# Kernel optimization log

Hardware: AMD Instinct MI355X
Metric: run time of the kernel (lower is better)

The kernel has to match this reference:

```python
import jax, jax.numpy as jnp
import numpy as np

K = 128   # per-head dim == input dim
H = 8     # heads
B = 2
T = 2048


def setup_inputs() -> dict:
    key = jax.random.key(0)
    ks = jax.random.split(key, 6)
    s_in = 1.0 / np.sqrt(K)
    s_out = 1.0 / np.sqrt(K * H)
    return {
        "x": jax.random.normal(ks[0], (B, T, K), dtype=jnp.float32),
        # Linear weights stored as (in, out); torch Linear init ~ U(-1/sqrt(in), 1/sqrt(in))
        "Wq": jax.random.uniform(ks[1], (K, K * H), jnp.float32, -s_in, s_in),
        "Wk": jax.random.uniform(ks[2], (K, K * H), jnp.float32, -s_in, s_in),
        "Wv": jax.random.uniform(ks[3], (K, K * H), jnp.float32, -s_in, s_in),
        "Wo": jax.random.uniform(ks[4], (K * H, K), jnp.float32, -s_out, s_out),
        "bo": jax.random.uniform(ks[5], (K,), jnp.float32, -s_out, s_out),
    }


def reference(x, Wq, Wk, Wv, Wo, bo):
    b, t, k = x.shape
    h = H
    scale = k ** 0.25
    # projections -> [b, t, h, k]
    q = (x @ Wq).reshape(b, t, h, k) / scale
    ke = (x @ Wk).reshape(b, t, h, k) / scale
    v = (x @ Wv).reshape(b, t, h, k)
    # scores: [b, h, t, t]
    scores = jnp.einsum('bihk,bjhk->bhij', q, ke)
    # causal mask: positions j > i get -inf (diagonal kept)
    causal = jnp.tril(jnp.ones((t, t), dtype=bool))
    scores = jnp.where(causal[None, None], scores, -jnp.inf)
    p = jax.nn.softmax(scores, axis=-1)
    out = jnp.einsum('bhij,bjhk->bihk', p, v).reshape(b, t, h * k)
    return out @ Wo + bo
```

## Files before the change

### kernel.cpp

```cpp
#include <hip/hip_runtime.h>

typedef __bf16 bf16;
typedef __bf16 bf16x4 __attribute__((ext_vector_type(4)));
typedef __bf16 bf16x8 __attribute__((ext_vector_type(8)));
typedef float f32x4 __attribute__((ext_vector_type(4)));

#define MFMA16(a, b, c) __builtin_amdgcn_mfma_f32_16x16x32_bf16((a), (b), (c), 0, 0, 0)

__device__ __forceinline__ int swz16(int r, int c) { return (c ^ (r & 15)); }
__device__ __forceinline__ int swz8(int r, int c) { return (c ^ (r & 7)); }

__global__ __launch_bounds__(256) void tr3_kernel(
    const float* __restrict__ Wq, const float* __restrict__ Wk,
    const float* __restrict__ Wv, bf16* __restrict__ outbase) {
  __shared__ bf16 tile[32][33];
  const int z = blockIdx.z;
  const float* ib = (z == 0) ? Wq : (z == 1) ? Wk : Wv;
  bf16* ob = outbase + (size_t)z * 131072;
  int r0 = blockIdx.x * 32, c0 = blockIdx.y * 32;
  int tx = threadIdx.x & 31, ty = threadIdx.x >> 5;
#pragma unroll
  for (int i = 0; i < 4; ++i) {
    int r = ty + i * 8;
    tile[r][tx] = (bf16)ib[(size_t)(r0 + r) * 1024 + (c0 + tx)];
  }
  __syncthreads();
#pragma unroll
  for (int i = 0; i < 4; ++i) {
    int r = ty + i * 8;
    ob[(size_t)(c0 + r) * 128 + (r0 + tx)] = tile[tx][r];
  }
}

__global__ __launch_bounds__(256) void trWo_kernel(
    const float* __restrict__ in, bf16* __restrict__ out) {
  __shared__ bf16 tile[32][33];
  int r0 = blockIdx.x * 32, c0 = blockIdx.y * 32;
  int tx = threadIdx.x & 31, ty = threadIdx.x >> 5;
#pragma unroll
  for (int i = 0; i < 4; ++i) {
    int r = ty + i * 8;
    tile[r][tx] = (bf16)in[(size_t)(r0 + r) * 128 + (c0 + tx)];
  }
  __syncthreads();
#pragma unroll
  for (int i = 0; i < 4; ++i) {
    int r = ty + i * 8;
    out[(size_t)(c0 + r) * 1024 + (r0 + tx)] = tile[tx][r];
  }
}

__global__ __launch_bounds__(256) void proj_gemm(
    const float* __restrict__ x, const bf16* __restrict__ Wqt,
    const bf16* __restrict__ Wkt, const bf16* __restrict__ Wvt,
    bf16* __restrict__ Qb, bf16* __restrict__ Kb, bf16* __restrict__ Vt) {
  __shared__ __align__(16) bf16 As[128 * 128];
  __shared__ __align__(16) bf16 Bs[128 * 128];
  const int mt = blockIdx.x;
  const int nt = blockIdx.y;
  const int matid = nt >> 3, h = nt & 7;
  const bf16* W = (matid == 0) ? Wqt : (matid == 1) ? Wkt : Wvt;
  const int tid = threadIdx.x;
  const bf16* sb = W + (size_t)h * 128 * 128;
#pragma unroll
  for (int i = 0; i < 8; ++i) {
    int c = tid + i * 256;
    int r = c >> 4, cc = c & 15;
    const f32x4* p = (const f32x4*)(x + (size_t)(mt * 128 + r) * 128 + cc * 8);
    f32x4 a = p[0], b = p[1];
    bf16x8 o;
#pragma unroll
    for (int j = 0; j < 4; ++j) { o[j] = (bf16)a[j]; o[4 + j] = (bf16)b[j]; }
    *(bf16x8*)&As[r * 128 + swz16(r, cc) * 8] = o;
  }
#pragma unroll
  for (int i = 0; i < 8; ++i) {
    int c = tid + i * 256;
    int r = c >> 4, cc = c & 15;
    *(bf16x8*)&Bs[r * 128 + swz16(r, cc) * 8] = *(const bf16x8*)(sb + (size_t)r * 128 + cc * 8);
  }
  __syncthreads();
  const int wave = tid >> 6, lane = tid & 63;
  const int wr = (wave >> 1) * 64, wc = (wave & 1) * 64;
  const int lr = lane & 15, lkb = lane >> 4;
  const f32x4 FZ = {0.f, 0.f, 0.f, 0.f};
  f32x4 acc[4][4];
#pragma unroll
  for (int mf = 0; mf < 4; ++mf)
#pragma unroll
    for (int nf = 0; nf < 4; ++nf) acc[mf][nf] = FZ;
  const bool qk = (matid < 2);
#pragma unroll
  for (int ks = 0; ks < 4; ++ks) {
    bf16x8 a[4], b[4];
#pragma unroll
    for (int mf = 0; mf < 4; ++mf) {
      int r = wr + mf * 16 + lr;
      a[mf] = *(const bf16x8*)&As[r * 128 + swz16(r, ks * 4 + lkb) * 8];
    }
#pragma unroll
    for (int nf = 0; nf < 4; ++nf) {
      int r = wc + nf * 16 + lr;
      b[nf] = *(const bf16x8*)&Bs[r * 128 + swz16(r, ks * 4 + lkb) * 8];
    }
    if (qk) {
#pragma unroll
      for (int mf = 0; mf < 4; ++mf)
#pragma unroll
        for (int nf = 0; nf < 4; ++nf) acc[mf][nf] = MFMA16(b[nf], a[mf], acc[mf][nf]);
    } else {
#pragma unroll
      for (int mf = 0; mf < 4; ++mf)
#pragma unroll
        for (int nf = 0; nf < 4; ++nf) acc[mf][nf] = MFMA16(a[mf], b[nf], acc[mf][nf]);
    }
  }
  const int rb = lkb * 4;
  if (qk) {
    bf16* Out = (matid == 0) ? Qb : Kb;
#pragma unroll
    for (int mf = 0; mf < 4; ++mf)
#pragma unroll
      for (int nf = 0; nf < 4; ++nf) {
        int m = mt * 128 + wr + mf * 16 + lr;
        int d0 = wc + nf * 16 + rb;
        int bb = m >> 11, t = m & 2047;
        bf16x4 vv;
#pragma unroll
        for (int r = 0; r < 4; ++r) vv[r] = (bf16)acc[mf][nf][r];
        *(bf16x4*)(Out + ((size_t)(bb * 8 + h) * 2048 + t) * 128 + d0) = vv;
      }
  } else {
#pragma unroll
    for (int mf = 0; mf < 4; ++mf)
#pragma unroll
      for (int nf = 0; nf < 4; ++nf) {
        int d = wc + nf * 16 + lr;
        int m0 = mt * 128 + wr + mf * 16 + rb;
        int bb = m0 >> 11, t0 = m0 & 2047;
        bf16x4 vv;
#pragma unroll
        for (int r = 0; r < 4; ++r) vv[r] = (bf16)acc[mf][nf][r];
        *(bf16x4*)(Vt + ((size_t)(bb * 8 + h) * 128 + d) * 2048 + t0) = vv;
      }
  }
}

__global__ __launch_bounds__(256, 3) void attn_kernel(
    bf16* __restrict__ Qb, const bf16* __restrict__ Kb, const bf16* __restrict__ Vt) {
  __shared__ __align__(16) bf16 Ks[64 * 128];
  __shared__ __align__(16) bf16 Vs[128 * 64];
  __shared__ __align__(16) bf16 Ps[4 * 16 * 64];
  const f32x4 FZ = {0.f, 0.f, 0.f, 0.f};
  const int bid = blockIdx.x;
  const int qt = 31 - (bid >> 4);
  const int bh = bid & 15;
  const int nT = qt + 1;
  const bf16* Qh = Qb + (size_t)bh * 2048 * 128;
  bf16* Qw = Qb + (size_t)bh * 2048 * 128;
  const bf16* Kh = Kb + (size_t)bh * 2048 * 128;
  const bf16* Vh = Vt + (size_t)bh * 128 * 2048;
  const int tid = threadIdx.x, wave = tid >> 6, lane = tid & 63;
  const int lr = lane & 15, lkb = lane >> 4, rb = lkb * 4;
  const float SCL = 0.12751744f;
  const int qrow = qt * 64 + wave * 16;

  const int krow = tid >> 4, kcc = tid & 15;
  bf16* kdst = &Ks[krow * 128 + (kcc ^ krow) * 8];
  const bf16* ksrc0 = Kh + (size_t)krow * 128 + kcc * 8;
  const int vrow = tid >> 3, vcc = tid & 7;
  bf16* vdst = &Vs[vrow * 64 + (vcc ^ (vrow & 7)) * 8];
  const bf16* vsrc0 = Vh + (size_t)vrow * 2048 + vcc * 8;

  float mrun[4], lrun[4];
  f32x4 O[8];
  bf16x8 qf[4];
#pragma unroll
  for (int r = 0; r < 4; ++r) { mrun[r] = -__builtin_inff(); lrun[r] = 0.f; }
#pragma unroll
  for (int nf = 0; nf < 8; ++nf) O[nf] = FZ;
#pragma unroll
  for (int ks = 0; ks < 4; ++ks)
    qf[ks] = *(const bf16x8*)(Qh + (size_t)(qrow + lr) * 128 + ks * 32 + lkb * 8);

  bf16x8 kpre[4], vpre[4];
#pragma unroll
  for (int i = 0; i < 4; ++i) kpre[i] = *(const bf16x8*)(ksrc0 + i * 2048);
#pragma unroll
  for (int i = 0; i < 4; ++i) vpre[i] = *(const bf16x8*)(vsrc0 + i * 65536);

  for (int it = 0; it < nT; ++it) {
    __syncthreads();
#pragma unroll
    for (int i = 0; i < 4; ++i) *(bf16x8*)(kdst + i * 2048) = kpre[i];
#pragma unroll
    for (int i = 0; i < 4; ++i) *(bf16x8*)(vdst + i * 2048) = vpre[i];
    __syncthreads();
    if (it + 1 < nT) {
      const size_t koff = (size_t)(it + 1) * 8192;
      const size_t voff = (size_t)(it + 1) * 64;
#pragma unroll
      for (int i = 0; i < 4; ++i) kpre[i] = *(const bf16x8*)(ksrc0 + koff + i * 2048);
#pragma unroll
      for (int i = 0; i < 4; ++i) vpre[i] = *(const bf16x8*)(vsrc0 + voff + i * 65536);
    }
    f32x4 s[4];
#pragma unroll
    for (int nf = 0; nf < 4; ++nf) s[nf] = FZ;
#pragma unroll
    for (int ks = 0; ks < 4; ++ks) {
#pragma unroll
      for (int nf = 0; nf < 4; ++nf) {
        int r = nf * 16 + lr;
        bf16x8 b = *(const bf16x8*)&Ks[r * 128 + swz16(r, ks * 4 + lkb) * 8];
        s[nf] = MFMA16(qf[ks], b, s[nf]);
      }
    }
    float pmax[4];
#pragma unroll
    for (int r = 0; r < 4; ++r) pmax[r] = -__builtin_inff();
    if (it == qt) {
#pragma unroll
      for (int nf = 0; nf < 4; ++nf) {
        int colg = (qt << 6) + nf * 16 + lr;
#pragma unroll
        for (int r = 0; r < 4; ++r) {
          int rowg = qrow + rb + r;
          float v = (colg > rowg) ? -__builtin_inff() : s[nf][r];
          s[nf][r] = v;
          pmax[r] = fmaxf(pmax[r], v);
        }
      }
    } else {
#pragma unroll
      for (int nf = 0; nf < 4; ++nf)
#pragma unroll
        for (int r = 0; r < 4; ++r) pmax[r] = fmaxf(pmax[r], s[nf][r]);
    }
#pragma unroll
    for (int r = 0; r < 4; ++r) {
      float v = pmax[r];
      v = fmaxf(v, __shfl_xor(v, 1, 64));
      v = fmaxf(v, __shfl_xor(v, 2, 64));
      v = fmaxf(v, __shfl_xor(v, 4, 64));
      v = fmaxf(v, __shfl_xor(v, 8, 64));
      pmax[r] = v;
    }
    float alpha[4];
#pragma unroll
    for (int r = 0; r < 4; ++r) {
      float mnew = fmaxf(mrun[r], pmax[r] * SCL);
      alpha[r] = exp2f(mrun[r] - mnew);
      mrun[r] = mnew;
    }
    float psum[4] = {0.f, 0.f, 0.f, 0.f};
#pragma unroll
    for (int nf = 0; nf < 4; ++nf)
#pragma unroll
      for (int r = 0; r < 4; ++r) {
        float p = exp2f(__builtin_fmaf(s[nf][r], SCL, -mrun[r]));
        s[nf][r] = p;
        psum[r] += p;
      }
#pragma unroll
    for (int r = 0; r < 4; ++r) {
      float v = psum[r];
      v += __shfl_xor(v, 1, 64);
      v += __shfl_xor(v, 2, 64);
      v += __shfl_xor(v, 4, 64);
      v += __shfl_xor(v, 8, 64);
      lrun[r] = lrun[r] * alpha[r] + v;
    }
#pragma unroll
    for (int nf = 0; nf < 8; ++nf) {
#pragma unroll
      for (int r = 0; r < 4; ++r) O[nf][r] *= alpha[r];
    }
#pragma unroll
    for (int nf = 0; nf < 4; ++nf) {
#pragma unroll
      for (int r = 0; r < 4; ++r) {
        int row = rb + r;
        int col = nf * 16 + lr;
        Ps[wave * 1024 + row * 64 + swz8(row, col >> 3) * 8 + (col & 7)] = (bf16)s[nf][r];
      }
    }
#pragma unroll
    for (int ks2 = 0; ks2 < 2; ++ks2) {
      bf16x8 a = *(const bf16x8*)&Ps[wave * 1024 + lr * 64 + swz8(lr, ks2 * 4 + lkb) * 8];
#pragma unroll
      for (int nf = 0; nf < 8; ++nf) {
        int r = nf * 16 + lr;
        bf16x8 b = *(const bf16x8*)&Vs[r * 64 + swz8(r, ks2 * 4 + lkb) * 8];
        O[nf] = MFMA16(a, b, O[nf]);
      }
    }
  }
#pragma unroll
  for (int r = 0; r < 4; ++r) {
    float inv = 1.f / lrun[r];
    int t = qrow + rb + r;
#pragma unroll
    for (int nf = 0; nf < 8; ++nf)
      Qw[(size_t)t * 128 + nf * 16 + lr] = (bf16)(O[nf][r] * inv);
  }
}

__global__ __launch_bounds__(256) void outproj_kernel(
    const bf16* __restrict__ AO, const bf16* __restrict__ Wot,
    const float* __restrict__ bo, float* __restrict__ out) {
  __shared__ __align__(16) bf16 As[32 * 128];
  __shared__ __align__(16) bf16 Bs[128 * 128];
  const f32x4 FZ = {0.f, 0.f, 0.f, 0.f};
  const int mt = blockIdx.x;
  const int tid = threadIdx.x, wave = tid >> 6, lane = tid & 63;
  const int lr = lane & 15, lkb = lane >> 4, rb = lkb * 4;
  const int wr = (wave >> 1) * 16, wc = (wave & 1) * 64;
  f32x4 acc[4];
#pragma unroll
  for (int nf = 0; nf < 4; ++nf) acc[nf] = FZ;
  for (int kt = 0; kt < 8; ++kt) {
    __syncthreads();
#pragma unroll
    for (int i = 0; i < 2; ++i) {
      int c = tid + i * 256;
      int r = c >> 4, cc = c & 15;
      int m = mt * 32 + r, bb = m >> 11, t = m & 2047;
      *(bf16x8*)&As[r * 128 + swz16(r, cc) * 8] =
          *(const bf16x8*)(AO + ((size_t)(bb * 8 + kt) * 2048 + t) * 128 + cc * 8);
    }
#pragma unroll
    for (int i = 0; i < 8; ++i) {
      int c = tid + i * 256;
      int r = c >> 4, cc = c & 15;
      *(bf16x8*)&Bs[r * 128 + swz16(r, cc) * 8] =
          *(const bf16x8*)(Wot + (size_t)r * 1024 + kt * 128 + cc * 8);
    }
    __syncthreads();
#pragma unroll
    for (int ks = 0; ks < 4; ++ks) {
      int ra = wr + lr;
      bf16x8 a = *(const bf16x8*)&As[ra * 128 + swz16(ra, ks * 4 + lkb) * 8];
#pragma unroll
      for (int nf = 0; nf < 4; ++nf) {
        int r = wc + nf * 16 + lr;
        bf16x8 b = *(const bf16x8*)&Bs[r * 128 + swz16(r, ks * 4 + lkb) * 8];
        acc[nf] = MFMA16(a, b, acc[nf]);
      }
    }
  }
#pragma unroll
  for (int nf = 0; nf < 4; ++nf)
#pragma unroll
    for (int r = 0; r < 4; ++r) {
      int m = mt * 32 + wr + rb + r;
      int n = wc + nf * 16 + lr;
      out[(size_t)m * 128 + n] = acc[nf][r] + bo[n];
    }
}

extern "C" void kernel_launch(void* const* d_in, const int* in_sizes, int n_in,
                              void* d_out, int out_size, void* d_ws, size_t ws_size,
                              hipStream_t stream) {
  (void)in_sizes; (void)n_in; (void)out_size; (void)ws_size;
  const float* x  = (const float*)d_in[0];
  const float* Wq = (const float*)d_in[1];
  const float* Wk = (const float*)d_in[2];
  const float* Wv = (const float*)d_in[3];
  const float* Wo = (const float*)d_in[4];
  const float* bo = (const float*)d_in[5];
  float* out = (float*)d_out;

  bf16* ws  = (bf16*)d_ws;
  bf16* Wqt = ws;
  bf16* Wkt = Wqt + 131072;
  bf16* Wvt = Wkt + 131072;
  bf16* Wot = Wvt + 131072;
  bf16* Qb  = Wot + 131072;
  bf16* Kb  = Qb + 4194304;
  bf16* Vt  = Kb + 4194304;

  tr3_kernel<<<dim3(4, 32, 3), 256, 0, stream>>>(Wq, Wk, Wv, Wqt);
  trWo_kernel<<<dim3(32, 4, 1), 256, 0, stream>>>(Wo, Wot);
  proj_gemm<<<dim3(32, 24, 1), 256, 0, stream>>>(x, Wqt, Wkt, Wvt, Qb, Kb, Vt);
  attn_kernel<<<dim3(512, 1, 1), 256, 0, stream>>>(Qb, Kb, Vt);
  outproj_kernel<<<dim3(128, 1, 1), 256, 0, stream>>>(Qb, Wot, bo, out);
}
```

Baseline: 159.8 us.

## Split attention KV range across two wave groups and merge softmax partials

The attention kernel now runs 512 threads per block as two groups of four waves. Each group processes half of the causal KV tiles with its own K/V shared buffers, and the partial O, m and l values are merged through shared memory at the end. This shortens the serial KV loop per block and evens out causal load imbalance, at the cost of 80KB of dynamic LDS, extra barriers and a merge step. The two weight-transpose kernels are also fused into one launch.

Measured after the change: 247.1 us. 1.55x slower.

```diff
diff --git a/kernel.cpp b/kernel.cpp
--- a/kernel.cpp
+++ b/kernel.cpp
@@ -10,43 +10,29 @@
 __device__ __forceinline__ int swz16(int r, int c) { return (c ^ (r & 15)); }
 __device__ __forceinline__ int swz8(int r, int c) { return (c ^ (r & 7)); }
 
-__global__ __launch_bounds__(256) void tr3_kernel(
+__global__ __launch_bounds__(256) void trW_kernel(
     const float* __restrict__ Wq, const float* __restrict__ Wk,
-    const float* __restrict__ Wv, bf16* __restrict__ outbase) {
+    const float* __restrict__ Wv, const float* __restrict__ Wo,
+    bf16* __restrict__ outbase) {
   __shared__ bf16 tile[32][33];
   const int z = blockIdx.z;
-  const float* ib = (z == 0) ? Wq : (z == 1) ? Wk : Wv;
+  const float* ib = (z == 0) ? Wq : (z == 1) ? Wk : (z == 2) ? Wv : Wo;
   bf16* ob = outbase + (size_t)z * 131072;
-  int r0 = blockIdx.x * 32, c0 = blockIdx.y * 32;
+  const int R = (z < 3) ? 128 : 1024;
+  const int C = (z < 3) ? 1024 : 128;
+  int r0 = (z < 3) ? blockIdx.y * 32 : blockIdx.x * 32;
+  int c0 = (z < 3) ? blockIdx.x * 32 : blockIdx.y * 32;
   int tx = threadIdx.x & 31, ty = threadIdx.x >> 5;
 #pragma unroll
   for (int i = 0; i < 4; ++i) {
     int r = ty + i * 8;
-    tile[r][tx] = (bf16)ib[(size_t)(r0 + r) * 1024 + (c0 + tx)];
+    tile[r][tx] = (bf16)ib[(size_t)(r0 + r) * C + (c0 + tx)];
   }
   __syncthreads();
 #pragma unroll
   for (int i = 0; i < 4; ++i) {
     int r = ty + i * 8;
-    ob[(size_t)(c0 + r) * 128 + (r0 + tx)] = tile[tx][r];
-  }
-}
-
-__global__ __launch_bounds__(256) void trWo_kernel(
-    const float* __restrict__ in, bf16* __restrict__ out) {
-  __shared__ bf16 tile[32][33];
-  int r0 = blockIdx.x * 32, c0 = blockIdx.y * 32;
-  int tx = threadIdx.x & 31, ty = threadIdx.x >> 5;
-#pragma unroll
-  for (int i = 0; i < 4; ++i) {
-    int r = ty + i * 8;
-    tile[r][tx] = (bf16)in[(size_t)(r0 + r) * 128 + (c0 + tx)];
-  }
-  __syncthreads();
-#pragma unroll
-  for (int i = 0; i < 4; ++i) {
-    int r = ty + i * 8;
-    out[(size_t)(c0 + r) * 1024 + (r0 + tx)] = tile[tx][r];
+    ob[(size_t)(c0 + r) * R + (r0 + tx)] = tile[tx][r];
   }
 }
 
@@ -146,29 +132,37 @@
   }
 }
 
-__global__ __launch_bounds__(256, 3) void attn_kernel(
+__global__ __launch_bounds__(512, 4) void attn_kernel(
     bf16* __restrict__ Qb, const bf16* __restrict__ Kb, const bf16* __restrict__ Vt) {
-  __shared__ __align__(16) bf16 Ks[64 * 128];
-  __shared__ __align__(16) bf16 Vs[128 * 64];
-  __shared__ __align__(16) bf16 Ps[4 * 16 * 64];
+  extern __shared__ char smem[];
   const f32x4 FZ = {0.f, 0.f, 0.f, 0.f};
   const int bid = blockIdx.x;
   const int qt = 31 - (bid >> 4);
   const int bh = bid & 15;
   const int nT = qt + 1;
+  const int h0 = (nT + 1) >> 1, h1 = nT - h0;
   const bf16* Qh = Qb + (size_t)bh * 2048 * 128;
   bf16* Qw = Qb + (size_t)bh * 2048 * 128;
   const bf16* Kh = Kb + (size_t)bh * 2048 * 128;
   const bf16* Vh = Vt + (size_t)bh * 128 * 2048;
   const int tid = threadIdx.x, wave = tid >> 6, lane = tid & 63;
+  const int g = tid >> 8;
+  const int tg = tid & 255;
+  const int gw = wave & 3;
   const int lr = lane & 15, lkb = lane >> 4, rb = lkb * 4;
   const float SCL = 0.12751744f;
-  const int qrow = qt * 64 + wave * 16;
-
-  const int krow = tid >> 4, kcc = tid & 15;
+  const int qrow = qt * 64 + gw * 16;
+  const int hg = g ? h1 : h0;
+  const int tbase = g ? h0 : 0;
+
+  bf16* Ks = (bf16*)(smem + g * 16384);
+  bf16* Vs = (bf16*)(smem + 32768 + g * 16384);
+  bf16* Ps = (bf16*)(smem + 65536) + wave * 1024;
+
+  const int krow = tg >> 4, kcc = tg & 15;
   bf16* kdst = &Ks[krow * 128 + (kcc ^ krow) * 8];
   const bf16* ksrc0 = Kh + (size_t)krow * 128 + kcc * 8;
-  const int vrow = tid >> 3, vcc = tid & 7;
+  const int vrow = tg >> 3, vcc = tg & 7;
   bf16* vdst = &Vs[vrow * 64 + (vcc ^ (vrow & 7)) * 8];
   const bf16* vsrc0 = Vh + (size_t)vrow * 2048 + vcc * 8;
 
@@ -184,26 +178,33 @@
     qf[ks] = *(const bf16x8*)(Qh + (size_t)(qrow + lr) * 128 + ks * 32 + lkb * 8);
 
   bf16x8 kpre[4], vpre[4];
-#pragma unroll
-  for (int i = 0; i < 4; ++i) kpre[i] = *(const bf16x8*)(ksrc0 + i * 2048);
-#pragma unroll
-  for (int i = 0; i < 4; ++i) vpre[i] = *(const bf16x8*)(vsrc0 + i * 65536);
-
-  for (int it = 0; it < nT; ++it) {
+  if (hg > 0) {
+    const size_t ko = (size_t)tbase * 8192, vo = (size_t)tbase * 64;
+#pragma unroll
+    for (int i = 0; i < 4; ++i) kpre[i] = *(const bf16x8*)(ksrc0 + ko + i * 2048);
+#pragma unroll
+    for (int i = 0; i < 4; ++i) vpre[i] = *(const bf16x8*)(vsrc0 + vo + i * 65536);
+  }
+
+  for (int it = 0; it < h0; ++it) {
+    const bool act = (it < hg);
+    const int kvt = tbase + it;
     __syncthreads();
-#pragma unroll
-    for (int i = 0; i < 4; ++i) *(bf16x8*)(kdst + i * 2048) = kpre[i];
-#pragma unroll
-    for (int i = 0; i < 4; ++i) *(bf16x8*)(vdst + i * 2048) = vpre[i];
+    if (act) {
+#pragma unroll
+      for (int i = 0; i < 4; ++i) *(bf16x8*)(kdst + i * 2048) = kpre[i];
+#pragma unroll
+      for (int i = 0; i < 4; ++i) *(bf16x8*)(vdst + i * 2048) = vpre[i];
+    }
     __syncthreads();
-    if (it + 1 < nT) {
-      const size_t koff = (size_t)(it + 1) * 8192;
-      const size_t voff = (size_t)(it + 1) * 64;
-#pragma unroll
-      for (int i = 0; i < 4; ++i) kpre[i] = *(const bf16x8*)(ksrc0 + koff + i * 2048);
-#pragma unroll
-      for (int i = 0; i < 4; ++i) vpre[i] = *(const bf16x8*)(vsrc0 + voff + i * 65536);
-    }
+    if (it + 1 < hg) {
+      const size_t ko = (size_t)(kvt + 1) * 8192, vo = (size_t)(kvt + 1) * 64;
+#pragma unroll
+      for (int i = 0; i < 4; ++i) kpre[i] = *(const bf16x8*)(ksrc0 + ko + i * 2048);
+#pragma unroll
+      for (int i = 0; i < 4; ++i) vpre[i] = *(const bf16x8*)(vsrc0 + vo + i * 65536);
+    }
+    if (!act) continue;
     f32x4 s[4];
 #pragma unroll
     for (int nf = 0; nf < 4; ++nf) s[nf] = FZ;
@@ -219,7 +220,7 @@
     float pmax[4];
 #pragma unroll
     for (int r = 0; r < 4; ++r) pmax[r] = -__builtin_inff();
-    if (it == qt) {
+    if (kvt == qt) {
 #pragma unroll
       for (int nf = 0; nf < 4; ++nf) {
         int colg = (qt << 6) + nf * 16 + lr;
@@ -282,12 +283,12 @@
       for (int r = 0; r < 4; ++r) {
         int row = rb + r;
         int col = nf * 16 + lr;
-        Ps[wave * 1024 + row * 64 + swz8(row, col >> 3) * 8 + (col & 7)] = (bf16)s[nf][r];
+        Ps[row * 64 + swz8(row, col >> 3) * 8 + (col & 7)] = (bf16)s[nf][r];
       }
     }
 #pragma unroll
     for (int ks2 = 0; ks2 < 2; ++ks2) {
-      bf16x8 a = *(const bf16x8*)&Ps[wave * 1024 + lr * 64 + swz8(lr, ks2 * 4 + lkb) * 8];
+      bf16x8 a = *(const bf16x8*)&Ps[lr * 64 + swz8(lr, ks2 * 4 + lkb) * 8];
 #pragma unroll
       for (int nf = 0; nf < 8; ++nf) {
         int r = nf * 16 + lr;
@@ -296,13 +297,42 @@
       }
     }
   }
-#pragma unroll
-  for (int r = 0; r < 4; ++r) {
-    float inv = 1.f / lrun[r];
-    int t = qrow + rb + r;
+
+  float* Om = (float*)smem;
+  float* Lm = (float*)(smem + 32768);
+  float* Ll = (float*)(smem + 33280);
+  __syncthreads();
+  if (g == 1) {
 #pragma unroll
     for (int nf = 0; nf < 8; ++nf)
-      Qw[(size_t)t * 128 + nf * 16 + lr] = (bf16)(O[nf][r] * inv);
+#pragma unroll
+      for (int r = 0; r < 4; ++r)
+        Om[(gw * 16 + rb + r) * 128 + nf * 16 + lr] = O[nf][r];
+    if (lr == 0) {
+#pragma unroll
+      for (int r = 0; r < 4; ++r) {
+        Lm[gw * 16 + rb + r] = mrun[r];
+        Ll[gw * 16 + rb + r] = lrun[r];
+      }
+    }
+  }
+  __syncthreads();
+  if (g == 0) {
+#pragma unroll
+    for (int r = 0; r < 4; ++r) {
+      int row = gw * 16 + rb + r;
+      float m1 = Lm[row], l1 = Ll[row];
+      float m = fmaxf(mrun[r], m1);
+      float a0 = exp2f(mrun[r] - m), a1 = exp2f(m1 - m);
+      float inv = 1.f / (lrun[r] * a0 + l1 * a1);
+      int t = qrow + rb + r;
+#pragma unroll
+      for (int nf = 0; nf < 8; ++nf) {
+        float o1 = Om[row * 128 + nf * 16 + lr];
+        Qw[(size_t)t * 128 + nf * 16 + lr] =
+            (bf16)((O[nf][r] * a0 + o1 * a1) * inv);
+      }
+    }
   }
 }
 
@@ -380,9 +410,8 @@
   bf16* Kb  = Qb + 4194304;
   bf16* Vt  = Kb + 4194304;
 
-  tr3_kernel<<<dim3(4, 32, 3), 256, 0, stream>>>(Wq, Wk, Wv, Wqt);
-  trWo_kernel<<<dim3(32, 4, 1), 256, 0, stream>>>(Wo, Wot);
+  trW_kernel<<<dim3(32, 4, 4), 256, 0, stream>>>(Wq, Wk, Wv, Wo, Wqt);
   proj_gemm<<<dim3(32, 24, 1), 256, 0, stream>>>(x, Wqt, Wkt, Wvt, Qb, Kb, Vt);
-  attn_kernel<<<dim3(512, 1, 1), 256, 0, stream>>>(Qb, Kb, Vt);
+  attn_kernel<<<dim3(512, 1, 1), 512, 81920, stream>>>(Qb, Kb, Vt);
   outproj_kernel<<<dim3(128, 1, 1), 256, 0, stream>>>(Qb, Wot, bo, out);
 }
```
